# Optimization experiments

Hardware: AMD Instinct MI355X
Metric: run time of the kernel (lower is better)

Reference implementation:

```python
import jax, jax.numpy as jnp
import numpy as np

B, T, C = 8, 2048, 1024
HEAD_SIZE = 64
HEAD_NUM = 0
NUM_HEADS = 16


def setup_inputs() -> dict:
    key = jax.random.key(0)
    k1, k2, k3, k4 = jax.random.split(key, 4)
    x = jax.random.normal(k1, (B, T, C), dtype=jnp.float32)
    s = C ** -0.5  # Linear init scale
    Wq = jax.random.normal(k2, (C, HEAD_SIZE), dtype=jnp.float32) * s
    Wk = jax.random.normal(k3, (C, HEAD_SIZE), dtype=jnp.float32) * s
    Wv = jax.random.normal(k4, (C, HEAD_SIZE), dtype=jnp.float32) * s
    return {"x": x, "Wq": Wq, "Wk": Wk, "Wv": Wv}


def reference(x, Wq, Wk, Wv):
    # single head of self-attention with ALiBi bias + causal mask (dropout in eval mode = identity)
    q = x @ Wq  # [B,T,H]
    k = x @ Wk  # [B,T,H]
    v = x @ Wv  # [B,T,H]
    scale = jnp.float32(HEAD_SIZE) ** -0.5
    t = jnp.arange(T)
    # base_bias[i,j] = j - i, scaled by per-head ALiBi slope
    slope = 2.0 ** (-8.0 * (HEAD_NUM + 1) / NUM_HEADS)
    m = (t[None, :] - t[:, None]).astype(jnp.float32) * slope  # [T,T]
    # note: bias is added BEFORE the 1/sqrt(d) scaling, as in the original
    scores = (jnp.einsum('bqh,bkh->bqk', q, k) + m) * scale  # [B,T,T]
    causal = t[None, :] <= t[:, None]  # [T,T] lower-triangular
    scores = jnp.where(causal, scores, -jnp.inf)
    attn = jax.nn.softmax(scores, axis=-1)
    out = jnp.einsum('bqk,bkh->bqh', attn, v)  # [B,T,H]
    return out
```

## Files before the change

kernel.cpp:

```cpp
#include <hip/hip_runtime.h>
#include <hip/hip_bf16.h>
#include <math.h>

#define B_ 8
#define T_ 2048
#define C_ 1024
#define H_ 64
#define M_ (B_*T_)

typedef __attribute__((ext_vector_type(8))) short bf16x8;
typedef __attribute__((ext_vector_type(4))) float floatx4;

static __device__ __forceinline__ unsigned short f2bf(float f) {
    union { float f; unsigned u; } v; v.f = f;
    unsigned r = v.u + 0x7fffu + ((v.u >> 16) & 1u);
    return (unsigned short)(r >> 16);
}
static __device__ __forceinline__ unsigned short f2bf_fast(float f) {
    union { float f; unsigned u; } v; v.f = f;
    return (unsigned short)((v.u + 0x8000u) >> 16);
}
static __device__ __forceinline__ unsigned pk2h(float lo, float hi) {
    union { float f; unsigned u; } a, b; a.f = lo; b.f = hi;
    return __builtin_amdgcn_perm(b.u + 0x8000u, a.u + 0x8000u, 0x07060302u);
}
static __device__ __forceinline__ bf16x8 cvt8(float4 f0, float4 f1) {
    union { uint4 u; bf16x8 v; } r;
    r.u.x = pk2h(f0.x, f0.y); r.u.y = pk2h(f0.z, f0.w);
    r.u.z = pk2h(f1.x, f1.y); r.u.w = pk2h(f1.z, f1.w);
    return r.v;
}

#define MFMA(a,b,c) __builtin_amdgcn_mfma_f32_16x16x32_bf16((a),(b),(c),0,0,0)

__global__ __launch_bounds__(256) void wprep_kernel(
    const float* __restrict__ Wq, const float* __restrict__ Wk,
    const float* __restrict__ Wv, unsigned short* __restrict__ wt2)
{
    const int f    = blockIdx.x * 256 + threadIdx.x;
    const int nt   = f >> 11;
    const int kc   = (f >> 6) & 31;
    const int lane = f & 63;
    const int l15  = lane & 15, quad = lane >> 4;
    const int col  = nt * 16 + l15;
    const float* W = (col < 64) ? Wq : ((col < 128) ? Wk : Wv);
    const int   cw = col & 63;
    const float sc = (col < 64) ? 0.125f : 1.0f;
    unsigned short o[8];
    #pragma unroll
    for (int j = 0; j < 8; j++) {
        const int kk = kc * 32 + quad * 8 + j;
        o[j] = f2bf(W[(size_t)kk * 64 + cw] * sc);
    }
    *(uint4*)&wt2[(size_t)f * 8] = *(const uint4*)o;
}

__global__ __launch_bounds__(256) void qkv_kernel(
    const float* __restrict__ x, const unsigned short* __restrict__ wt2,
    unsigned short* __restrict__ qo, unsigned short* __restrict__ ko,
    unsigned short* __restrict__ vo)
{
    __shared__ __align__(16) unsigned short smem[64 * 200];
    #define XS_(buf) (smem + (buf) * 4608)

    const int t    = threadIdx.x;
    const int w    = t >> 6;
    const int lane = t & 63;
    const int l15  = lane & 15;
    const int quad = lane >> 4;
    const int r0   = blockIdx.x * 64;

    const int srow = t >> 2;
    const int g0   = t & 3;
    const float* xrow = x + (size_t)(r0 + srow) * C_;

    const unsigned short* wb = wt2 + (size_t)(w * 3) * 32 * 512 + lane * 8;

    floatx4 acc[4][3];
    #pragma unroll
    for (int mt = 0; mt < 4; mt++)
        #pragma unroll
        for (int nt = 0; nt < 3; nt++) acc[mt][nt] = (floatx4)(0.0f);

    float4 xA[4], xB[4];
    bf16x8 wcur[6], wnxt[6];

    #pragma unroll
    for (int j = 0; j < 2; j++) {
        const int g = g0 + 4 * j;
        xA[2*j+0] = *(const float4*)(xrow + g * 8);
        xA[2*j+1] = *(const float4*)(xrow + g * 8 + 4);
        xB[2*j+0] = *(const float4*)(xrow + 64 + g * 8);
        xB[2*j+1] = *(const float4*)(xrow + 64 + g * 8 + 4);
    }
    #pragma unroll
    for (int nt = 0; nt < 3; nt++)
        #pragma unroll
        for (int ks = 0; ks < 2; ks++)
            wcur[nt * 2 + ks] = *(const bf16x8*)(wb + (size_t)(nt * 32 + ks) * 512);
    #pragma unroll
    for (int j = 0; j < 2; j++) {
        const int g = g0 + 4 * j;
        *(bf16x8*)(XS_(0) + srow * 72 + g * 8) = cvt8(xA[2*j], xA[2*j+1]);
    }
    __syncthreads();

    #define QSTEP(c, Xcur, Xnext, buf)                                         \
    {                                                                          \
        if ((c) < 14) {                                                        \
            const int k2 = ((c) + 2) * 64;                                     \
            _Pragma("unroll")                                                  \
            for (int j = 0; j < 2; j++) {                                      \
                const int g = g0 + 4 * j;                                      \
                Xcur[2*j+0] = *(const float4*)(xrow + k2 + g * 8);             \
                Xcur[2*j+1] = *(const float4*)(xrow + k2 + g * 8 + 4);         \
            }                                                                  \
        }                                                                      \
        if ((c) < 15) {                                                        \
            _Pragma("unroll")                                                  \
            for (int nt = 0; nt < 3; nt++)                                     \
                _Pragma("unroll")                                              \
                for (int ks = 0; ks < 2; ks++)                                 \
                    wnxt[nt * 2 + ks] = *(const bf16x8*)                       \
                        (wb + (size_t)(nt * 32 + 2 * ((c) + 1) + ks) * 512);   \
        }                                                                      \
        _Pragma("unroll")                                                      \
        for (int ks = 0; ks < 2; ks++) {                                       \
            bf16x8 af[4];                                                      \
            _Pragma("unroll")                                                  \
            for (int mt = 0; mt < 4; mt++)                                     \
                af[mt] = *(const bf16x8*)                                      \
                    (XS_(buf) + (mt * 16 + l15) * 72 + ks * 32 + quad * 8);    \
            _Pragma("unroll")                                                  \
            for (int mt = 0; mt < 4; mt++)                                     \
                _Pragma("unroll")                                              \
                for (int nt = 0; nt < 3; nt++)                                 \
                    acc[mt][nt] = MFMA(af[mt], wcur[nt * 2 + ks], acc[mt][nt]);\
        }                                                                      \
        if ((c) < 15) {                                                        \
            _Pragma("unroll")                                                  \
            for (int j = 0; j < 2; j++) {                                      \
                const int g = g0 + 4 * j;                                      \
                *(bf16x8*)(XS_((buf) ^ 1) + srow * 72 + g * 8)                 \
                    = cvt8(Xnext[2*j], Xnext[2*j+1]);                          \
            }                                                                  \
            _Pragma("unroll")                                                  \
            for (int i = 0; i < 6; i++) wcur[i] = wnxt[i];                     \
        }                                                                      \
        __syncthreads();                                                       \
    }

    for (int cc = 0; cc < 16; cc += 2) {
        QSTEP(cc,     xA, xB, 0)
        QSTEP(cc + 1, xB, xA, 1)
    }
    #undef QSTEP

    #pragma unroll
    for (int mt = 0; mt < 4; mt++)
        #pragma unroll
        for (int nt = 0; nt < 3; nt++) {
            const int col = w * 48 + nt * 16 + l15;
            #pragma unroll
            for (int r = 0; r < 4; r++)
                smem[(mt * 16 + quad * 4 + r) * 200 + col] = f2bf(acc[mt][nt][r]);
        }
    __syncthreads();

    {
        #pragma unroll
        for (int i = 0; i < 2; i++) {
            const int fo  = t + i * 256;
            const int row = fo >> 3;
            const int oct = fo & 7;
            *(uint4*)&qo[(size_t)(r0 + row) * 64 + oct * 8] =
                *(const uint4*)&smem[row * 200 + oct * 8];
            *(uint4*)&ko[(size_t)(r0 + row) * 64 + oct * 8] =
                *(const uint4*)&smem[row * 200 + 64 + oct * 8];
        }
    }
    {
        const int h = t >> 2, ts = (t & 3) * 16;
        const int bb = r0 >> 11, tt = r0 & 2047;
        unsigned short tmp[16];
        #pragma unroll
        for (int j = 0; j < 16; j++) tmp[j] = smem[(ts + j) * 200 + 128 + h];
        #pragma unroll
        for (int j = 0; j < 2; j++)
            *(uint4*)&vo[((size_t)bb * 64 + h) * 2048 + tt + ts + j * 8] =
                *(uint4*)&tmp[j * 8];
    }
    #undef XS_
}

__global__ __launch_bounds__(256, 2) void attn_kernel(
    const unsigned short* __restrict__ q,
    const unsigned short* __restrict__ k,
    const unsigned short* __restrict__ vT,
    float* __restrict__ out)
{
    __shared__ __align__(16) unsigned char smem[32768 + 1024];
    unsigned short* pT  = (unsigned short*)smem;
    float*          Omg = (float*)smem;
    float*          mlg = (float*)(smem + 32768);

    const int t    = threadIdx.x;
    const int w    = t >> 6;
    const int lane = t & 63;
    const int l15  = lane & 15;
    const int quad = lane >> 4;
    const int b    = blockIdx.x & 7;
    const int qt   = 63 - (blockIdx.x >> 3);
    const int q0   = qt * 32;
    const size_t kb = (size_t)b * T_ * 64;

    bf16x8 qf[2][2];
    #pragma unroll
    for (int rt = 0; rt < 2; rt++)
        #pragma unroll
        for (int ks = 0; ks < 2; ks++)
            qf[rt][ks] = *(const bf16x8*)
                &q[kb + (size_t)(q0 + rt * 16 + l15) * 64 + ks * 32 + quad * 8];

    floatx4 O[2][4];
    float mrow[2][4], lrow[2][4], igb[2][4];
    const float bs = 0.088388347648318447f;
    #pragma unroll
    for (int rt = 0; rt < 2; rt++) {
        #pragma unroll
        for (int nt = 0; nt < 4; nt++) O[rt][nt] = (floatx4)(0.0f);
        #pragma unroll
        for (int r = 0; r < 4; r++) {
            mrow[rt][r] = -INFINITY; lrow[rt][r] = 0.0f;
            igb[rt][r] = (float)(q0 + rt * 16 + quad * 4 + r) * bs;
        }
    }

    const int nsteps = (q0 + 32 + 63) >> 6;
    const int ns4    = (nsteps + 3) >> 2;
    const int sBeg   = w * ns4;
    const int sEnd   = min(sBeg + ns4, nsteps);
    unsigned short* pw = pT + w * 32 * 72;

    bf16x8 kf[4][2], vf[4][2];
    #define LOADK(dK, jj0)                                                     \
        { _Pragma("unroll")                                                    \
          for (int nt = 0; nt < 4; nt++)                                       \
              _Pragma("unroll")                                                \
              for (int ks = 0; ks < 2; ks++)                                   \
                  dK[nt][ks] = *(const bf16x8*)                                \
                      &k[kb + (size_t)((jj0) + nt*16 + l15)*64 + ks*32 + quad*8]; }
    #define LOADV(dV, jj0)                                                     \
        { _Pragma("unroll")                                                    \
          for (int nt = 0; nt < 4; nt++)                                       \
              _Pragma("unroll")                                                \
              for (int ks = 0; ks < 2; ks++)                                   \
                  dV[nt][ks] = *(const bf16x8*)                                \
                      &vT[((size_t)b*64 + nt*16 + l15)*2048 + (jj0) + ks*32 + quad*8]; }

    if (sBeg < sEnd) LOADK(kf, sBeg * 64)

    for (int s = sBeg; s < sEnd; s++) {
        const int j0 = s * 64;

        floatx4 sc[2][4];
        #pragma unroll
        for (int rt = 0; rt < 2; rt++)
            #pragma unroll
            for (int nt = 0; nt < 4; nt++) {
                floatx4 z = (floatx4)(0.0f);
                z = MFMA(qf[rt][0], kf[nt][0], z);
                z = MFMA(qf[rt][1], kf[nt][1], z);
                sc[rt][nt] = z;
            }

        LOADV(vf, j0)
        bf16x8 kf2[4][2];
        const bool more = (s + 1 < sEnd);
        if (more) LOADK(kf2, (s + 1) * 64)

        const float jbase = (float)(j0 + l15) * bs;
        #pragma unroll
        for (int rt = 0; rt < 2; rt++)
            #pragma unroll
            for (int r = 0; r < 4; r++) {
                const int   ig = q0 + rt * 16 + quad * 4 + r;
                const float c0 = jbase - igb[rt][r];
                float xv[4];
                float mloc = -INFINITY;
                #pragma unroll
                for (int nt = 0; nt < 4; nt++) {
                    const int j = j0 + nt * 16 + l15;
                    float v2 = (sc[rt][nt][r] + c0) + (float)(nt * 16) * bs;
                    if (j > ig) v2 = -INFINITY;
                    xv[nt] = v2;
                    mloc = fmaxf(mloc, v2);
                }
                #pragma unroll
                for (int off = 1; off < 16; off <<= 1)
                    mloc = fmaxf(mloc, __shfl_xor(mloc, off));
                const float mnew = fmaxf(mrow[rt][r], mloc);
                const float mq   = (mnew == -INFINITY) ? 0.0f : mnew;
                const float alpha = __expf(mrow[rt][r] - mq);
                mrow[rt][r] = mnew;
                float ps = 0.0f;
                #pragma unroll
                for (int nt = 0; nt < 4; nt++) {
                    const float p = __expf(xv[nt] - mq);
                    ps += p;
                    pw[(rt * 16 + quad * 4 + r) * 72 + nt * 16 + l15] = f2bf_fast(p);
                }
                lrow[rt][r] = lrow[rt][r] * alpha + ps;
                #pragma unroll
                for (int nt = 0; nt < 4; nt++) O[rt][nt][r] *= alpha;
            }

        #pragma unroll
        for (int rt = 0; rt < 2; rt++) {
            const bf16x8 pf0 = *(const bf16x8*)&pw[(rt * 16 + l15) * 72 + quad * 8];
            const bf16x8 pf1 = *(const bf16x8*)&pw[(rt * 16 + l15) * 72 + 32 + quad * 8];
            #pragma unroll
            for (int nt = 0; nt < 4; nt++) {
                O[rt][nt] = MFMA(pf0, vf[nt][0], O[rt][nt]);
                O[rt][nt] = MFMA(pf1, vf[nt][1], O[rt][nt]);
            }
        }

        if (more) {
            #pragma unroll
            for (int nt = 0; nt < 4; nt++)
                #pragma unroll
                for (int ks = 0; ks < 2; ks++)
                    kf[nt][ks] = kf2[nt][ks];
        }
    }
    #undef LOADK
    #undef LOADV

    #pragma unroll
    for (int rt = 0; rt < 2; rt++)
        #pragma unroll
        for (int r = 0; r < 4; r++)
            #pragma unroll
            for (int off = 1; off < 16; off <<= 1)
                lrow[rt][r] += __shfl_xor(lrow[rt][r], off);

    __syncthreads();

    #pragma unroll
    for (int rt = 0; rt < 2; rt++)
        #pragma unroll
        for (int nt = 0; nt < 4; nt++)
            #pragma unroll
            for (int r = 0; r < 4; r++)
                Omg[w * 2048 + (rt * 16 + quad * 4 + r) * 64 + nt * 16 + l15]
                    = O[rt][nt][r];
    if (l15 == 0) {
        #pragma unroll
        for (int rt = 0; rt < 2; rt++)
            #pragma unroll
            for (int r = 0; r < 4; r++) {
                mlg[w * 64 + rt * 16 + quad * 4 + r]      = mrow[rt][r];
                mlg[w * 64 + 32 + rt * 16 + quad * 4 + r] = lrow[rt][r];
            }
    }
    __syncthreads();

    {
        const int row = t >> 3;
        const int hq  = (t & 7) << 3;
        float mstar = -INFINITY;
        #pragma unroll
        for (int w2 = 0; w2 < 4; w2++)
            mstar = fmaxf(mstar, mlg[w2 * 64 + row]);
        floatx4 oa0 = (floatx4)(0.0f), oa1 = (floatx4)(0.0f);
        float lsum = 0.0f;
        #pragma unroll
        for (int w2 = 0; w2 < 4; w2++) {
            const float wg = __expf(mlg[w2 * 64 + row] - mstar);
            lsum += wg * mlg[w2 * 64 + 32 + row];
            oa0 += wg * *(const floatx4*)&Omg[w2 * 2048 + row * 64 + hq];
            oa1 += wg * *(const floatx4*)&Omg[w2 * 2048 + row * 64 + hq + 4];
        }
        const float inv = 1.0f / lsum;
        *(floatx4*)&out[kb + (size_t)(q0 + row) * 64 + hq]     = oa0 * inv;
        *(floatx4*)&out[kb + (size_t)(q0 + row) * 64 + hq + 4] = oa1 * inv;
    }
}

extern "C" void kernel_launch(void* const* d_in, const int* in_sizes, int n_in,
                              void* d_out, int out_size, void* d_ws, size_t ws_size,
                              hipStream_t stream) {
    (void)in_sizes; (void)n_in; (void)out_size; (void)ws_size;
    const float* x  = (const float*)d_in[0];
    const float* Wq = (const float*)d_in[1];
    const float* Wk = (const float*)d_in[2];
    const float* Wv = (const float*)d_in[3];
    float* out = (float*)d_out;

    unsigned short* wt2 = (unsigned short*)d_ws;
    unsigned short* qw  = wt2 + 196608;
    unsigned short* kw  = qw + (size_t)M_ * H_;
    unsigned short* vw  = kw + (size_t)M_ * H_;

    wprep_kernel<<<96, 256, 0, stream>>>(Wq, Wk, Wv, wt2);
    qkv_kernel<<<M_ / 64, 256, 0, stream>>>(x, wt2, qw, kw, vw);
    attn_kernel<<<B_ * 64, 256, 0, stream>>>(qw, kw, vw, out);
}
```

Baseline: 140.5 us.

## Halve QKV projection row tile and drop K prefetch to raise attention occupancy

The QKV projection kernel now handles 32 rows per block instead of 64, doubling the grid to 512 blocks so more CUs have work, at the cost of reloading the weights twice as often. The attention kernel drops its register double-buffered K prefetch and loads K and V inside the loop, and raises launch bounds to 3 blocks per CU. This trades load-latency hiding for lower register pressure and higher occupancy.

Measured after the change: 144.3 us. 2.7% more time.

```diff
diff --git a/kernel.cpp b/kernel.cpp
--- a/kernel.cpp
+++ b/kernel.cpp
@@ -60,61 +60,49 @@
     unsigned short* __restrict__ qo, unsigned short* __restrict__ ko,
     unsigned short* __restrict__ vo)
 {
-    __shared__ __align__(16) unsigned short smem[64 * 200];
-    #define XS_(buf) (smem + (buf) * 4608)
+    __shared__ __align__(16) unsigned short smem[32 * 200];
+    #define XS_(buf) (smem + (buf) * 2304)
 
     const int t    = threadIdx.x;
     const int w    = t >> 6;
     const int lane = t & 63;
     const int l15  = lane & 15;
     const int quad = lane >> 4;
-    const int r0   = blockIdx.x * 64;
-
-    const int srow = t >> 2;
-    const int g0   = t & 3;
+    const int r0   = blockIdx.x * 32;
+
+    const int srow = t >> 3;
+    const int g0   = t & 7;
     const float* xrow = x + (size_t)(r0 + srow) * C_;
 
     const unsigned short* wb = wt2 + (size_t)(w * 3) * 32 * 512 + lane * 8;
 
-    floatx4 acc[4][3];
-    #pragma unroll
-    for (int mt = 0; mt < 4; mt++)
+    floatx4 acc[2][3];
+    #pragma unroll
+    for (int mt = 0; mt < 2; mt++)
         #pragma unroll
         for (int nt = 0; nt < 3; nt++) acc[mt][nt] = (floatx4)(0.0f);
 
-    float4 xA[4], xB[4];
+    float4 xA[2], xB[2];
     bf16x8 wcur[6], wnxt[6];
 
-    #pragma unroll
-    for (int j = 0; j < 2; j++) {
-        const int g = g0 + 4 * j;
-        xA[2*j+0] = *(const float4*)(xrow + g * 8);
-        xA[2*j+1] = *(const float4*)(xrow + g * 8 + 4);
-        xB[2*j+0] = *(const float4*)(xrow + 64 + g * 8);
-        xB[2*j+1] = *(const float4*)(xrow + 64 + g * 8 + 4);
-    }
+    xA[0] = *(const float4*)(xrow + g0 * 8);
+    xA[1] = *(const float4*)(xrow + g0 * 8 + 4);
+    xB[0] = *(const float4*)(xrow + 64 + g0 * 8);
+    xB[1] = *(const float4*)(xrow + 64 + g0 * 8 + 4);
     #pragma unroll
     for (int nt = 0; nt < 3; nt++)
         #pragma unroll
         for (int ks = 0; ks < 2; ks++)
             wcur[nt * 2 + ks] = *(const bf16x8*)(wb + (size_t)(nt * 32 + ks) * 512);
-    #pragma unroll
-    for (int j = 0; j < 2; j++) {
-        const int g = g0 + 4 * j;
-        *(bf16x8*)(XS_(0) + srow * 72 + g * 8) = cvt8(xA[2*j], xA[2*j+1]);
-    }
+    *(bf16x8*)(XS_(0) + srow * 72 + g0 * 8) = cvt8(xA[0], xA[1]);
     __syncthreads();
 
     #define QSTEP(c, Xcur, Xnext, buf)                                         \
     {                                                                          \
         if ((c) < 14) {                                                        \
             const int k2 = ((c) + 2) * 64;                                     \
-            _Pragma("unroll")                                                  \
-            for (int j = 0; j < 2; j++) {                                      \
-                const int g = g0 + 4 * j;                                      \
-                Xcur[2*j+0] = *(const float4*)(xrow + k2 + g * 8);             \
-                Xcur[2*j+1] = *(const float4*)(xrow + k2 + g * 8 + 4);         \
-            }                                                                  \
+            Xcur[0] = *(const float4*)(xrow + k2 + g0 * 8);                    \
+            Xcur[1] = *(const float4*)(xrow + k2 + g0 * 8 + 4);                \
         }                                                                      \
         if ((c) < 15) {                                                        \
             _Pragma("unroll")                                                  \
@@ -126,24 +114,20 @@
         }                                                                      \
         _Pragma("unroll")                                                      \
         for (int ks = 0; ks < 2; ks++) {                                       \
-            bf16x8 af[4];                                                      \
+            bf16x8 af[2];                                                      \
             _Pragma("unroll")                                                  \
-            for (int mt = 0; mt < 4; mt++)                                     \
+            for (int mt = 0; mt < 2; mt++)                                     \
                 af[mt] = *(const bf16x8*)                                      \
                     (XS_(buf) + (mt * 16 + l15) * 72 + ks * 32 + quad * 8);    \
             _Pragma("unroll")                                                  \
-            for (int mt = 0; mt < 4; mt++)                                     \
+            for (int mt = 0; mt < 2; mt++)                                     \
                 _Pragma("unroll")                                              \
                 for (int nt = 0; nt < 3; nt++)                                 \
                     acc[mt][nt] = MFMA(af[mt], wcur[nt * 2 + ks], acc[mt][nt]);\
         }                                                                      \
         if ((c) < 15) {                                                        \
-            _Pragma("unroll")                                                  \
-            for (int j = 0; j < 2; j++) {                                      \
-                const int g = g0 + 4 * j;                                      \
-                *(bf16x8*)(XS_((buf) ^ 1) + srow * 72 + g * 8)                 \
-                    = cvt8(Xnext[2*j], Xnext[2*j+1]);                          \
-            }                                                                  \
+            *(bf16x8*)(XS_((buf) ^ 1) + srow * 72 + g0 * 8)                    \
+                = cvt8(Xnext[0], Xnext[1]);                                    \
             _Pragma("unroll")                                                  \
             for (int i = 0; i < 6; i++) wcur[i] = wnxt[i];                     \
         }                                                                      \
@@ -157,7 +141,7 @@
     #undef QSTEP
 
     #pragma unroll
-    for (int mt = 0; mt < 4; mt++)
+    for (int mt = 0; mt < 2; mt++)
         #pragma unroll
         for (int nt = 0; nt < 3; nt++) {
             const int col = w * 48 + nt * 16 + l15;
@@ -168,32 +152,25 @@
     __syncthreads();
 
     {
-        #pragma unroll
-        for (int i = 0; i < 2; i++) {
-            const int fo  = t + i * 256;
-            const int row = fo >> 3;
-            const int oct = fo & 7;
-            *(uint4*)&qo[(size_t)(r0 + row) * 64 + oct * 8] =
-                *(const uint4*)&smem[row * 200 + oct * 8];
-            *(uint4*)&ko[(size_t)(r0 + row) * 64 + oct * 8] =
-                *(const uint4*)&smem[row * 200 + 64 + oct * 8];
-        }
+        const int row = t >> 3, oct = t & 7;
+        *(uint4*)&qo[(size_t)(r0 + row) * 64 + oct * 8] =
+            *(const uint4*)&smem[row * 200 + oct * 8];
+        *(uint4*)&ko[(size_t)(r0 + row) * 64 + oct * 8] =
+            *(const uint4*)&smem[row * 200 + 64 + oct * 8];
     }
     {
-        const int h = t >> 2, ts = (t & 3) * 16;
+        const int h  = t >> 2;
+        const int j0 = (t & 3) * 8;
         const int bb = r0 >> 11, tt = r0 & 2047;
-        unsigned short tmp[16];
-        #pragma unroll
-        for (int j = 0; j < 16; j++) tmp[j] = smem[(ts + j) * 200 + 128 + h];
-        #pragma unroll
-        for (int j = 0; j < 2; j++)
-            *(uint4*)&vo[((size_t)bb * 64 + h) * 2048 + tt + ts + j * 8] =
-                *(uint4*)&tmp[j * 8];
+        unsigned short tmp[8];
+        #pragma unroll
+        for (int j = 0; j < 8; j++) tmp[j] = smem[(j0 + j) * 200 + 128 + h];
+        *(uint4*)&vo[((size_t)bb * 64 + h) * 2048 + tt + j0] = *(uint4*)tmp;
     }
     #undef XS_
 }
 
-__global__ __launch_bounds__(256, 2) void attn_kernel(
+__global__ __launch_bounds__(256, 3) void attn_kernel(
     const unsigned short* __restrict__ q,
     const unsigned short* __restrict__ k,
     const unsigned short* __restrict__ vT,
@@ -242,26 +219,16 @@
     const int sEnd   = min(sBeg + ns4, nsteps);
     unsigned short* pw = pT + w * 32 * 72;
 
-    bf16x8 kf[4][2], vf[4][2];
-    #define LOADK(dK, jj0)                                                     \
-        { _Pragma("unroll")                                                    \
-          for (int nt = 0; nt < 4; nt++)                                       \
-              _Pragma("unroll")                                                \
-              for (int ks = 0; ks < 2; ks++)                                   \
-                  dK[nt][ks] = *(const bf16x8*)                                \
-                      &k[kb + (size_t)((jj0) + nt*16 + l15)*64 + ks*32 + quad*8]; }
-    #define LOADV(dV, jj0)                                                     \
-        { _Pragma("unroll")                                                    \
-          for (int nt = 0; nt < 4; nt++)                                       \
-              _Pragma("unroll")                                                \
-              for (int ks = 0; ks < 2; ks++)                                   \
-                  dV[nt][ks] = *(const bf16x8*)                                \
-                      &vT[((size_t)b*64 + nt*16 + l15)*2048 + (jj0) + ks*32 + quad*8]; }
-
-    if (sBeg < sEnd) LOADK(kf, sBeg * 64)
-
     for (int s = sBeg; s < sEnd; s++) {
         const int j0 = s * 64;
+
+        bf16x8 kf[4][2];
+        #pragma unroll
+        for (int nt = 0; nt < 4; nt++)
+            #pragma unroll
+            for (int ks = 0; ks < 2; ks++)
+                kf[nt][ks] = *(const bf16x8*)
+                    &k[kb + (size_t)(j0 + nt * 16 + l15) * 64 + ks * 32 + quad * 8];
 
         floatx4 sc[2][4];
         #pragma unroll
@@ -274,10 +241,13 @@
                 sc[rt][nt] = z;
             }
 
-        LOADV(vf, j0)
-        bf16x8 kf2[4][2];
-        const bool more = (s + 1 < sEnd);
-        if (more) LOADK(kf2, (s + 1) * 64)
+        bf16x8 vf[4][2];
+        #pragma unroll
+        for (int nt = 0; nt < 4; nt++)
+            #pragma unroll
+            for (int ks = 0; ks < 2; ks++)
+                vf[nt][ks] = *(const bf16x8*)
+                    &vT[((size_t)b * 64 + nt * 16 + l15) * 2048 + j0 + ks * 32 + quad * 8];
 
         const float jbase = (float)(j0 + l15) * bs;
         #pragma unroll
@@ -325,17 +295,7 @@
                 O[rt][nt] = MFMA(pf1, vf[nt][1], O[rt][nt]);
             }
         }
-
-        if (more) {
-            #pragma unroll
-            for (int nt = 0; nt < 4; nt++)
-                #pragma unroll
-                for (int ks = 0; ks < 2; ks++)
-                    kf[nt][ks] = kf2[nt][ks];
-        }
-    }
-    #undef LOADK
-    #undef LOADV
+    }
 
     #pragma unroll
     for (int rt = 0; rt < 2; rt++)
@@ -404,6 +364,6 @@
     unsigned short* vw  = kw + (size_t)M_ * H_;
 
     wprep_kernel<<<96, 256, 0, stream>>>(Wq, Wk, Wv, wt2);
-    qkv_kernel<<<M_ / 64, 256, 0, stream>>>(x, wt2, qw, kw, vw);
+    qkv_kernel<<<M_ / 32, 256, 0, stream>>>(x, wt2, qw, kw, vw);
     attn_kernel<<<B_ * 64, 256, 0, stream>>>(qw, kw, vw, out);
 }
```
